# Kernel tuning notes

Hardware: AMD Instinct MI355X
Metric: run time of the kernel (lower is better)

## Reference

```python
import jax, jax.numpy as jnp
import numpy as np

B, N, C, NS = 4, 2048, 128, 64
RADIUS = 0.25
BN_EPS = 1e-5


def _ball_query(xyz):
    """First-NS point indices within RADIUS of each point (pointnet2 semantics:
    indices taken in ascending point order, short balls padded with the first hit).
    xyz: (B,N,3) -> idx: (B,N,NS) int32."""
    sq = jnp.sum(xyz * xyz, axis=-1)                                   # (B,N)
    d2 = sq[:, :, None] + sq[:, None, :] - 2.0 * jnp.einsum('bnd,bmd->bnm', xyz, xyz)
    within = d2 < RADIUS ** 2                                          # (B,N,N)
    cand = jnp.where(within, jnp.arange(N, dtype=jnp.int32)[None, None, :], N)
    idx = jnp.sort(cand, axis=-1)[..., :NS]                            # first NS hits
    idx = jnp.where(idx == N, idx[..., :1], idx)                       # pad with first hit
    return idx


def _bn_relu(h, g, b):
    # eval-mode BatchNorm2d with running_mean=0, running_var=1, then ReLU
    inv = 1.0 / jnp.sqrt(1.0 + BN_EPS)
    return jax.nn.relu(g[None, :, None, None] * (h * inv) + b[None, :, None, None])


def _forward(xyz, features, W1, W2, W3, g1, g2, g3, b1, b2, b3):
    idx = _ball_query(xyz)                                             # (B,N,NS)
    bidx = jnp.arange(B)[:, None, None]
    g_xyz = xyz[bidx, idx]                                             # (B,N,NS,3)
    grouped_xyz = jnp.transpose(g_xyz - xyz[:, :, None, :], (0, 3, 1, 2))  # (B,3,N,NS) relative
    feat_t = jnp.transpose(features, (0, 2, 1))                        # (B,N,C)
    g_feat = jnp.transpose(feat_t[bidx, idx], (0, 3, 1, 2))            # (B,C,N,NS)
    grouped_features = jnp.concatenate([grouped_xyz, g_feat], axis=1)  # (B,3+C,N,NS)

    xyz_feature = jnp.concatenate([jnp.transpose(xyz, (0, 2, 1)), features], axis=1)  # (B,3+C,N)
    center = jax.lax.stop_gradient(xyz_feature)[..., None]             # .detach() in torch
    diff = grouped_features - center
    h = diff * diff                                                    # squared diff

    h = _bn_relu(jnp.einsum('oc,bcns->bons', W1, h), g1, b1)           # (B,256,N,NS)
    h = _bn_relu(jnp.einsum('oc,bcns->bons', W2, h), g2, b2)           # (B,128,N,NS)
    h = _bn_relu(jnp.einsum('oc,bcns->bons', W3, h), g3, b3)           # (B,1,N,NS)

    shift = jnp.sum(grouped_xyz * h, axis=-1)                          # (B,3,N)
    return shift / jnp.sum(h, axis=-1)                                 # / (B,1,N)


def setup_inputs() -> dict:
    key = jax.random.key(0)
    ks = jax.random.split(key, 5)
    cin = C + 3
    return {
        'xyz': jax.random.uniform(ks[0], (B, N, 3), dtype=jnp.float32),
        'features': jax.random.normal(ks[1], (B, C, N), dtype=jnp.float32),
        'W1': jax.random.normal(ks[2], (256, cin), dtype=jnp.float32) * np.float32(np.sqrt(2.0 / cin)),
        'W2': jax.random.normal(ks[3], (128, 256), dtype=jnp.float32) * np.float32(np.sqrt(2.0 / 256)),
        'W3': jax.random.normal(ks[4], (1, 128), dtype=jnp.float32) * np.float32(np.sqrt(2.0 / 128)),
        'g1': jnp.ones((256,), jnp.float32), 'g2': jnp.ones((128,), jnp.float32), 'g3': jnp.ones((1,), jnp.float32),
        'b1': jnp.zeros((256,), jnp.float32), 'b2': jnp.zeros((128,), jnp.float32), 'b3': jnp.zeros((1,), jnp.float32),
    }


def reference(xyz, features, W1, W2, W3, g1, g2, g3, b1, b2, b3):
    return _forward(xyz, features, W1, W2, W3, g1, g2, g3, b1, b2, b3)
```

## Files before the change

kernel.cpp:

```cpp
#include <hip/hip_runtime.h>
#include <math.h>

typedef _Float16 f16;
typedef _Float16 f16x8 __attribute__((ext_vector_type(8)));
typedef _Float16 f16x4 __attribute__((ext_vector_type(4)));
typedef float f32x4 __attribute__((ext_vector_type(4)));

#define B_  4
#define N_  2048
#define C_  128
#define NS_ 64

#define WS_FEAT16 0u
#define WS_IDX    2097152u
#define WS_W1X    3145728u
#define WS_W1P    3153920u
#define WS_W2P    3219456u

#define OFF_H   0
#define OFF_HX  16384
#define OFF_W   18432
#define OFF_GX  51200
#define OFF_Z3  51968
#define LDS_TOTAL 53248

__device__ __forceinline__ void gl_lds16(const char* gp, char* lp) {
  __builtin_amdgcn_global_load_lds(
      (const __attribute__((address_space(1))) unsigned int*)gp,
      (__attribute__((address_space(3))) unsigned int*)lp, 16, 0, 0);
}

__device__ __forceinline__ unsigned pk2(float a, float b) {
  union { f16 h[2]; unsigned u; } cv;
  cv.h[0] = (f16)a; cv.h[1] = (f16)b;
  return cv.u;
}

__global__ __launch_bounds__(256) void prep_kernel(
    const float* __restrict__ feat, const float* __restrict__ W1,
    const float* __restrict__ W2,
    const float* __restrict__ g1, const float* __restrict__ g2,
    f16* __restrict__ feat16,
    char* __restrict__ W1x, char* __restrict__ W1p, char* __restrict__ W2p)
{
  const float inv = 1.0f / sqrtf(1.0f + 1e-5f);
  int i = blockIdx.x * 256 + threadIdx.x;
  {
    int n = i & (N_ - 1);
    int bc = i >> 11;
    int c = bc & (C_ - 1);
    int b = bc >> 7;
    feat16[(size_t)((b << 11) + n) * C_ + c] = (f16)feat[i];
  }
  if (i < 16384) {
    int g = i >> 12, r = i & 4095, o = r >> 4, j = r & 15;
    float sc = g1[o] * inv;
    const float* row = W1 + o * 131 + 3 + g * 32 + 2 * j;
    unsigned byte = ((unsigned)(o * 64 + j * 4)) ^ ((unsigned)(((o >> 1) & 7) << 4));
    *(unsigned*)(W1p + (size_t)g * 16384 + byte) = pk2(row[0] * sc, row[1] * sc);
  }
  if (i < 16384) {
    int ko = i >> 12, r = i & 4095, p = r >> 5, j = r & 31;
    float sc = g2[p] * inv;
    int o = ko * 64 + 2 * j;
    unsigned byte = ((unsigned)(p * 128 + j * 4)) ^ ((unsigned)((p & 7) << 4));
    *(unsigned*)(W2p + (size_t)ko * 16384 + byte) =
        pk2(W2[p * 256 + o] * sc, W2[p * 256 + o + 1] * sc);
  }
  if (i < 2048) {
    int o = i >> 3, j = i & 7;
    float sc = g1[o] * inv;
    unsigned v = 0;
    if (j == 0)      v = pk2(W1[o * 131 + 0] * sc, W1[o * 131 + 1] * sc);
    else if (j == 1) v = pk2(W1[o * 131 + 2] * sc, 0.0f);
    *(unsigned*)(W1x + o * 32 + j * 4) = v;
  }
}

__global__ __launch_bounds__(256) void ballquery_kernel(
    const float* __restrict__ xyz, unsigned short* __restrict__ idxout)
{
  __shared__ float  xl[N_ * 3];
  __shared__ double sq[N_];
  __shared__ int    ibuf[4][NS_];

  const int b  = blockIdx.x >> 9;
  const int ng = blockIdx.x & 511;
  const int t  = threadIdx.x;
  const float* xb = xyz + (size_t)b * N_ * 3;

  for (int i = t; i < N_ * 3; i += 256) xl[i] = xb[i];
  __syncthreads();
  for (int i = t; i < N_; i += 256) {
    double x = (double)xl[3*i], y = (double)xl[3*i+1], z = (double)xl[3*i+2];
    sq[i] = x*x + y*y + z*z;
  }
  __syncthreads();

  const int wv = t >> 6, lane = t & 63;
  const int n = ng * 4 + wv;
  const double xn = (double)xl[3*n], yn = (double)xl[3*n+1], zn = (double)xl[3*n+2];
  const double sn = sq[n];

  int cnt = 0;
  for (int mb = 0; mb < N_; mb += 64) {
    int m = mb + lane;
    double dot = xn*(double)xl[3*m] + yn*(double)xl[3*m+1] + zn*(double)xl[3*m+2];
    double d2 = (sn + sq[m]) - 2.0 * dot;
    bool hit = d2 < 0.0625;
    unsigned long long mask = __ballot(hit);
    int pos = __popcll(mask & ((1ULL << lane) - 1ULL));
    int slot = cnt + pos;
    if (hit && slot < NS_) ibuf[wv][slot] = m;
    cnt += (int)__popcll(mask);
    if (cnt >= NS_) break;
  }
  asm volatile("s_waitcnt lgkmcnt(0)" ::: "memory");
  int total = cnt < NS_ ? cnt : NS_;
  int v = ibuf[wv][lane < total ? lane : 0];
  idxout[((size_t)b * N_ + n) * NS_ + lane] = (unsigned short)v;
}

__global__ __launch_bounds__(256, 3) void mlp_kernel(
    const float* __restrict__ xyz, const f16* __restrict__ feat16,
    const char* __restrict__ w1x, const char* __restrict__ w1p,
    const char* __restrict__ w2p,
    const unsigned short* __restrict__ idxg,
    const float* __restrict__ W3g,
    const float* __restrict__ b1,
    const float* __restrict__ b2,
    const float* __restrict__ g3, const float* __restrict__ b3,
    float* __restrict__ out)
{
  __shared__ __attribute__((aligned(128))) char lds[LDS_TOTAL];

  const int bidRaw = blockIdx.x;
  const int bn = ((bidRaw & 7) << 10) + (bidRaw >> 3);
  const int b = bn >> 11;
  const int n = bn & (N_ - 1);
  const int t = threadIdx.x;
  const int w = t >> 6, lane = t & 63;
  const int l15 = lane & 15, lg = lane >> 4;
  const unsigned swzl = (unsigned)(((l15 >> 1) & 7) << 4);
  const unsigned labase = ((unsigned)(l15 * 64 + lg * 16)) ^ swzl;
  const unsigned swz2 = (unsigned)((l15 & 7) << 4);
  const unsigned w2b0 = ((unsigned)(l15 * 128 + lg * 16)) ^ swz2;
  const unsigned w2b1 = ((unsigned)(l15 * 128 + 64 + lg * 16)) ^ swz2;
  const float inv = 1.0f / sqrtf(1.0f + 1e-5f);

  float bo1v[4];
  #pragma unroll
  for (int nt = 0; nt < 4; ++nt) {
    int o = (nt >> 1) * 128 + 32 * w + (nt & 1) * 16 + l15;
    bo1v[nt] = b1[o];
  }
  float bo2v[2];
  #pragma unroll
  for (int nt = 0; nt < 2; ++nt) {
    int p = 32 * w + nt * 16 + l15;
    bo2v[nt] = b2[p];
  }
  const float g3c = g3[0] * inv, b3c = b3[0];
  const float w3a = W3g[32 * w + l15] * g3c;
  const float w3b = W3g[32 * w + 16 + l15] * g3c;
  const float xn0 = xyz[(size_t)bn*3+0], xn1 = xyz[(size_t)bn*3+1], xn2 = xyz[(size_t)bn*3+2];

  auto STAGE = [&](int sl) {
    const char* gp; int nloads;
    if (sl == 0)      { gp = w1x;                          nloads = 2; }
    else if (sl <= 4) { gp = w1p + (size_t)(sl - 1) * 16384; nloads = 4; }
    else              { gp = w2p + (size_t)(sl - 5) * 16384; nloads = 4; }
    gp += t * 16;
    char* lp = lds + OFF_W + ((sl & 1) << 14) + (w << 10);
    for (int i = 0; i < nloads; ++i)
      gl_lds16(gp + i * 4096, lp + i * 4096);
  };

  f32x4 acc1[4][4];
  f32x4 acc2[4][2];
  #pragma unroll
  for (int mt = 0; mt < 4; ++mt)
    #pragma unroll
    for (int nt2 = 0; nt2 < 2; ++nt2) {
      f32x4 c = {bo2v[nt2], bo2v[nt2], bo2v[nt2], bo2v[nt2]};
      acc2[mt][nt2] = c;
    }

  STAGE(0);
  const int s_me = t & 63, g_me = t >> 6;
  const int m_me = (int)idxg[(size_t)bn * 64 + s_me];

  {
    const f16* pb = feat16 + ((size_t)b * N_ + m_me) * C_ + g_me * 32;
    const f16* qb = feat16 + (size_t)bn * C_ + g_me * 32;
    const unsigned sw = ((unsigned)((s_me >> 1) & 7)) << 4;
    const unsigned base = (unsigned)(g_me * 4096);
    #pragma unroll
    for (int qq = 0; qq < 4; ++qq) {
      f16x8 p = *(const f16x8*)(pb + qq * 8);
      f16x8 q = *(const f16x8*)(qb + qq * 8);
      f16x8 d = p - q;
      f16x8 hh = d * d;
      unsigned byte = base
        + ((((unsigned)(s_me * 64 + qq * 16)) ^ sw ^ ((unsigned)((g_me & 3) << 4))));
      *(f16x8*)(lds + OFF_H + byte) = hh;
    }
  }
  if (t < 64) {
    const float* pm = xyz + ((size_t)b * N_ + m_me) * 3;
    float p0 = pm[0], p1 = pm[1], p2c = pm[2];
    float* gxp = (float*)(lds + OFF_GX) + s_me * 3;
    gxp[0] = p0 - xn0; gxp[1] = p1 - xn1; gxp[2] = p2c - xn2;
    float h0 = p0 - 2.0f * xn0; h0 *= h0;
    float h1 = p1 - 2.0f * xn1; h1 *= h1;
    float h2 = p2c - 2.0f * xn2; h2 *= h2;
    char* hx = lds + OFF_HX + s_me * 32;
    *(unsigned*)(hx + 0)  = pk2(h0, h1);
    *(unsigned*)(hx + 4)  = pk2(h2, 0.0f);
    *(unsigned*)(hx + 8)  = 0u;
    *(unsigned*)(hx + 12) = 0u;
    f32x4 z4 = {0.0f, 0.0f, 0.0f, 0.0f};
    *(f32x4*)(hx + 16) = z4;
  }

  asm volatile("s_waitcnt vmcnt(0) lgkmcnt(0)" ::: "memory");
  __builtin_amdgcn_s_barrier();
  STAGE(1);
  {
    const char* wbx = lds + OFF_W;
    f16x4 bf4[4];
    #pragma unroll
    for (int nt = 0; nt < 4; ++nt) {
      int orow = (nt >> 1) * 128 + 32 * w + (nt & 1) * 16 + l15;
      bf4[nt] = *(const f16x4*)(wbx + orow * 32 + lg * 8);
    }
    f16x4 af4[4];
    #pragma unroll
    for (int mt = 0; mt < 4; ++mt)
      af4[mt] = *(const f16x4*)(lds + OFF_HX + (16 * mt + l15) * 32 + lg * 8);
    #pragma unroll
    for (int mt = 0; mt < 4; ++mt)
      #pragma unroll
      for (int nt = 0; nt < 4; ++nt) {
        f32x4 cb = {bo1v[nt], bo1v[nt], bo1v[nt], bo1v[nt]};
        acc1[mt][nt] = __builtin_amdgcn_mfma_f32_16x16x16f16(af4[mt], bf4[nt], cb, 0, 0, 0);
      }
  }

  #pragma unroll
  for (int g = 0; g < 4; ++g) {
    const int sl = 1 + g;
    asm volatile("s_waitcnt vmcnt(0) lgkmcnt(0)" ::: "memory");
    __builtin_amdgcn_s_barrier();
    STAGE(sl + 1);
    const char* wb = lds + OFF_W + ((sl & 1) << 14);
    f16x8 bf[4];
    #pragma unroll
    for (int nt = 0; nt < 4; ++nt) {
      int ob = (nt >> 1) * 128 + 32 * w + (nt & 1) * 16;
      bf[nt] = *(const f16x8*)(wb + ob * 64 + labase);
    }
    const char* hb = lds + OFF_H + g * 4096;
    const unsigned gx4 = ((unsigned)g) << 4;
    f16x8 af[4];
    #pragma unroll
    for (int mt = 0; mt < 4; ++mt)
      af[mt] = *(const f16x8*)(hb + mt * 1024 + (labase ^ gx4));
    __builtin_amdgcn_s_setprio(1);
    #pragma unroll
    for (int mt = 0; mt < 4; ++mt)
      #pragma unroll
      for (int nt = 0; nt < 4; ++nt)
        acc1[mt][nt] = __builtin_amdgcn_mfma_f32_16x16x32_f16(af[mt], bf[nt], acc1[mt][nt], 0, 0, 0);
    __builtin_amdgcn_s_setprio(0);
  }

  auto EPI1 = [&](int hf) {
    #pragma unroll
    for (int mt = 0; mt < 4; ++mt)
      #pragma unroll
      for (int nt2 = 0; nt2 < 2; ++nt2) {
        const int nt = hf * 2 + nt2;
        #pragma unroll
        for (int r = 0; r < 4; ++r) {
          int s = mt * 16 + lg * 4 + r;
          float a = acc1[mt][nt][r];
          a = a > 0.0f ? a : 0.0f;
          unsigned byte = (unsigned)(w * 4096)
            + (((unsigned)(s * 64 + nt2 * 32 + l15 * 2)) ^ ((unsigned)(((s >> 1) & 7) << 4))
               ^ ((unsigned)((w & 3) << 4)));
          *(f16*)(lds + OFF_H + byte) = (f16)a;
        }
      }
  };
  asm volatile("s_waitcnt lgkmcnt(0)" ::: "memory");
  __builtin_amdgcn_s_barrier();
  EPI1(0);

  #pragma unroll
  for (int k = 0; k < 4; ++k) {
    const int sl = 5 + k;
    asm volatile("s_waitcnt vmcnt(0) lgkmcnt(0)" ::: "memory");
    __builtin_amdgcn_s_barrier();
    if (sl < 8) STAGE(sl + 1);
    const char* wb = lds + OFF_W + ((sl & 1) << 14);
    f16x8 bq0[2], bq1[2];
    #pragma unroll
    for (int nt2 = 0; nt2 < 2; ++nt2) {
      int pb = (32 * w + nt2 * 16) * 128;
      bq0[nt2] = *(const f16x8*)(wb + pb + w2b0);
      bq1[nt2] = *(const f16x8*)(wb + pb + w2b1);
    }
    const int sl0 = (2 * k) & 3, sl1 = (2 * k + 1) & 3;
    f16x8 a0f[4], a1f[4];
    #pragma unroll
    for (int mt = 0; mt < 4; ++mt) {
      a0f[mt] = *(const f16x8*)(lds + OFF_H + sl0 * 4096 + mt * 1024 + (labase ^ (unsigned)(sl0 << 4)));
      a1f[mt] = *(const f16x8*)(lds + OFF_H + sl1 * 4096 + mt * 1024 + (labase ^ (unsigned)(sl1 << 4)));
    }
    __builtin_amdgcn_s_setprio(1);
    #pragma unroll
    for (int mt = 0; mt < 4; ++mt)
      #pragma unroll
      for (int nt2 = 0; nt2 < 2; ++nt2) {
        f32x4 c = acc2[mt][nt2];
        c = __builtin_amdgcn_mfma_f32_16x16x32_f16(a0f[mt], bq0[nt2], c, 0, 0, 0);
        c = __builtin_amdgcn_mfma_f32_16x16x32_f16(a1f[mt], bq1[nt2], c, 0, 0, 0);
        acc2[mt][nt2] = c;
      }
    __builtin_amdgcn_s_setprio(0);
    if (k == 1) {
      asm volatile("s_waitcnt lgkmcnt(0)" ::: "memory");
      __builtin_amdgcn_s_barrier();
      EPI1(1);
    }
  }

  {
    float pz[4][4];
    #pragma unroll
    for (int mt = 0; mt < 4; ++mt)
      #pragma unroll
      for (int r = 0; r < 4; ++r) {
        float a0 = acc2[mt][0][r]; a0 = a0 > 0.0f ? a0 : 0.0f;
        float a1 = acc2[mt][1][r]; a1 = a1 > 0.0f ? a1 : 0.0f;
        pz[mt][r] = fmaf(a0, w3a, a1 * w3b);
      }
    #pragma unroll
    for (int off = 1; off < 16; off <<= 1)
      #pragma unroll
      for (int mt = 0; mt < 4; ++mt)
        #pragma unroll
        for (int r = 0; r < 4; ++r)
          pz[mt][r] += __shfl_xor(pz[mt][r], off);
    if (l15 == 0) {
      float* z3p = (float*)(lds + OFF_Z3) + w * 64;
      #pragma unroll
      for (int mt = 0; mt < 4; ++mt)
        #pragma unroll
        for (int r = 0; r < 4; ++r)
          z3p[mt * 16 + lg * 4 + r] = pz[mt][r];
    }
  }
  asm volatile("s_waitcnt lgkmcnt(0)" ::: "memory");
  __builtin_amdgcn_s_barrier();

  if (t < 64) {
    const float* z3p = (const float*)(lds + OFF_Z3);
    float z3 = z3p[t] + z3p[64 + t] + z3p[128 + t] + z3p[192 + t] + b3c;
    float wgt = z3 > 0.0f ? z3 : 0.0f;
    const float* gx = (const float*)(lds + OFF_GX) + t * 3;
    float v0 = gx[0] * wgt, v1 = gx[1] * wgt, v2 = gx[2] * wgt, v3 = wgt;
    #pragma unroll
    for (int off = 1; off < 64; off <<= 1) {
      v0 += __shfl_xor(v0, off); v1 += __shfl_xor(v1, off);
      v2 += __shfl_xor(v2, off); v3 += __shfl_xor(v3, off);
    }
    if (t == 0) {
      out[(size_t)(b * 3 + 0) * N_ + n] = v0 / v3;
      out[(size_t)(b * 3 + 1) * N_ + n] = v1 / v3;
      out[(size_t)(b * 3 + 2) * N_ + n] = v2 / v3;
    }
  }
}

extern "C" void kernel_launch(void* const* d_in, const int* in_sizes, int n_in,
                              void* d_out, int out_size, void* d_ws, size_t ws_size,
                              hipStream_t stream) {
  (void)in_sizes; (void)n_in; (void)out_size; (void)ws_size;
  const float* xyz      = (const float*)d_in[0];
  const float* features = (const float*)d_in[1];
  const float* W1 = (const float*)d_in[2];
  const float* W2 = (const float*)d_in[3];
  const float* W3 = (const float*)d_in[4];
  const float* g1 = (const float*)d_in[5];
  const float* g2 = (const float*)d_in[6];
  const float* g3 = (const float*)d_in[7];
  const float* b1 = (const float*)d_in[8];
  const float* b2 = (const float*)d_in[9];
  const float* b3 = (const float*)d_in[10];
  float* out = (float*)d_out;

  char* ws = (char*)d_ws;
  f16* feat16         = (f16*)(ws + WS_FEAT16);
  unsigned short* idx = (unsigned short*)(ws + WS_IDX);
  char* W1x           = ws + WS_W1X;
  char* W1p           = ws + WS_W1P;
  char* W2p           = ws + WS_W2P;

  prep_kernel<<<dim3((B_ * C_ * N_) / 256), dim3(256), 0, stream>>>(
      features, W1, W2, g1, g2, feat16, W1x, W1p, W2p);
  ballquery_kernel<<<dim3(B_ * N_ / 4), dim3(256), 0, stream>>>(xyz, idx);
  mlp_kernel<<<dim3(B_ * N_), dim3(256), 0, stream>>>(
      xyz, feat16, W1x, W1p, W2p, idx, W3, b1, b2, g3, b3, out);
}
```

Baseline: 143.9 us.

## Make MLP kernel persistent with all weights resident in LDS

```diff
diff --git a/kernel.cpp b/kernel.cpp
--- a/kernel.cpp
+++ b/kernel.cpp
@@ -17,12 +17,14 @@
 #define WS_W1P    3153920u
 #define WS_W2P    3219456u
 
-#define OFF_H   0
-#define OFF_HX  16384
-#define OFF_W   18432
-#define OFF_GX  51200
-#define OFF_Z3  51968
-#define LDS_TOTAL 53248
+#define OFF_H    0
+#define OFF_HX   16384
+#define OFF_W1X  18432
+#define OFF_W1F  26624
+#define OFF_W2   92160
+#define OFF_GX   157696
+#define OFF_Z3   158464
+#define LDS_TOTAL 159488
 
 __device__ __forceinline__ void gl_lds16(const char* gp, char* lp) {
   __builtin_amdgcn_global_load_lds(
@@ -121,7 +123,7 @@
   idxout[((size_t)b * N_ + n) * NS_ + lane] = (unsigned short)v;
 }
 
-__global__ __launch_bounds__(256, 3) void mlp_kernel(
+__global__ __launch_bounds__(256, 1) void mlp_kernel(
     const float* __restrict__ xyz, const f16* __restrict__ feat16,
     const char* __restrict__ w1x, const char* __restrict__ w1p,
     const char* __restrict__ w2p,
@@ -134,10 +136,9 @@
 {
   __shared__ __attribute__((aligned(128))) char lds[LDS_TOTAL];
 
-  const int bidRaw = blockIdx.x;
-  const int bn = ((bidRaw & 7) << 10) + (bidRaw >> 3);
-  const int b = bn >> 11;
-  const int n = bn & (N_ - 1);
+  const int bid = blockIdx.x;
+  const int b = bid >> 6;
+  const int n0 = (bid & 63) * 32;
   const int t = threadIdx.x;
   const int w = t >> 6, lane = t & 63;
   const int l15 = lane & 15, lg = lane >> 4;
@@ -147,6 +148,7 @@
   const unsigned w2b0 = ((unsigned)(l15 * 128 + lg * 16)) ^ swz2;
   const unsigned w2b1 = ((unsigned)(l15 * 128 + 64 + lg * 16)) ^ swz2;
   const float inv = 1.0f / sqrtf(1.0f + 1e-5f);
+  const int s_me = t & 63, g_me = t >> 6;
 
   float bo1v[4];
   #pragma unroll
@@ -163,223 +165,267 @@
   const float g3c = g3[0] * inv, b3c = b3[0];
   const float w3a = W3g[32 * w + l15] * g3c;
   const float w3b = W3g[32 * w + 16 + l15] * g3c;
-  const float xn0 = xyz[(size_t)bn*3+0], xn1 = xyz[(size_t)bn*3+1], xn2 = xyz[(size_t)bn*3+2];
-
-  auto STAGE = [&](int sl) {
-    const char* gp; int nloads;
-    if (sl == 0)      { gp = w1x;                          nloads = 2; }
-    else if (sl <= 4) { gp = w1p + (size_t)(sl - 1) * 16384; nloads = 4; }
-    else              { gp = w2p + (size_t)(sl - 5) * 16384; nloads = 4; }
-    gp += t * 16;
-    char* lp = lds + OFF_W + ((sl & 1) << 14) + (w << 10);
-    for (int i = 0; i < nloads; ++i)
-      gl_lds16(gp + i * 4096, lp + i * 4096);
-  };
-
-  f32x4 acc1[4][4];
-  f32x4 acc2[4][2];
-  #pragma unroll
-  for (int mt = 0; mt < 4; ++mt)
-    #pragma unroll
-    for (int nt2 = 0; nt2 < 2; ++nt2) {
-      f32x4 c = {bo2v[nt2], bo2v[nt2], bo2v[nt2], bo2v[nt2]};
-      acc2[mt][nt2] = c;
-    }
-
-  STAGE(0);
-  const int s_me = t & 63, g_me = t >> 6;
-  const int m_me = (int)idxg[(size_t)bn * 64 + s_me];
 
   {
-    const f16* pb = feat16 + ((size_t)b * N_ + m_me) * C_ + g_me * 32;
+    #pragma unroll
+    for (int i2 = 0; i2 < 2; ++i2)
+      gl_lds16(w1x + (size_t)i2 * 4096 + t * 16, lds + OFF_W1X + i2 * 4096 + (w << 10));
+    #pragma unroll
+    for (int i2 = 0; i2 < 16; ++i2)
+      gl_lds16(w1p + (size_t)i2 * 4096 + t * 16, lds + OFF_W1F + i2 * 4096 + (w << 10));
+    #pragma unroll
+    for (int i2 = 0; i2 < 16; ++i2)
+      gl_lds16(w2p + (size_t)i2 * 4096 + t * 16, lds + OFF_W2 + i2 * 4096 + (w << 10));
+  }
+
+  f16x8 pf[4], qf_[4];
+  float pm0 = 0.f, pm1 = 0.f, pm2 = 0.f, xq0 = 0.f, xq1 = 0.f, xq2 = 0.f;
+
+  {
+    const int bn = b * N_ + n0;
+    const int m = (int)idxg[(size_t)bn * 64 + s_me];
+    const f16* pb = feat16 + ((size_t)b * N_ + m) * C_ + g_me * 32;
     const f16* qb = feat16 + (size_t)bn * C_ + g_me * 32;
     const unsigned sw = ((unsigned)((s_me >> 1) & 7)) << 4;
-    const unsigned base = (unsigned)(g_me * 4096);
     #pragma unroll
     for (int qq = 0; qq < 4; ++qq) {
       f16x8 p = *(const f16x8*)(pb + qq * 8);
       f16x8 q = *(const f16x8*)(qb + qq * 8);
       f16x8 d = p - q;
       f16x8 hh = d * d;
-      unsigned byte = base
+      unsigned byte = (unsigned)(g_me * 4096)
         + ((((unsigned)(s_me * 64 + qq * 16)) ^ sw ^ ((unsigned)((g_me & 3) << 4))));
       *(f16x8*)(lds + OFF_H + byte) = hh;
     }
-  }
-  if (t < 64) {
-    const float* pm = xyz + ((size_t)b * N_ + m_me) * 3;
-    float p0 = pm[0], p1 = pm[1], p2c = pm[2];
-    float* gxp = (float*)(lds + OFF_GX) + s_me * 3;
-    gxp[0] = p0 - xn0; gxp[1] = p1 - xn1; gxp[2] = p2c - xn2;
-    float h0 = p0 - 2.0f * xn0; h0 *= h0;
-    float h1 = p1 - 2.0f * xn1; h1 *= h1;
-    float h2 = p2c - 2.0f * xn2; h2 *= h2;
-    char* hx = lds + OFF_HX + s_me * 32;
-    *(unsigned*)(hx + 0)  = pk2(h0, h1);
-    *(unsigned*)(hx + 4)  = pk2(h2, 0.0f);
-    *(unsigned*)(hx + 8)  = 0u;
-    *(unsigned*)(hx + 12) = 0u;
-    f32x4 z4 = {0.0f, 0.0f, 0.0f, 0.0f};
-    *(f32x4*)(hx + 16) = z4;
-  }
-
-  asm volatile("s_waitcnt vmcnt(0) lgkmcnt(0)" ::: "memory");
-  __builtin_amdgcn_s_barrier();
-  STAGE(1);
-  {
-    const char* wbx = lds + OFF_W;
-    f16x4 bf4[4];
-    #pragma unroll
-    for (int nt = 0; nt < 4; ++nt) {
-      int orow = (nt >> 1) * 128 + 32 * w + (nt & 1) * 16 + l15;
-      bf4[nt] = *(const f16x4*)(wbx + orow * 32 + lg * 8);
-    }
-    f16x4 af4[4];
+    if (t < 64) {
+      float xn0c = xyz[(size_t)bn*3+0], xn1c = xyz[(size_t)bn*3+1], xn2c = xyz[(size_t)bn*3+2];
+      const float* pm = xyz + ((size_t)b * N_ + m) * 3;
+      float p0 = pm[0], p1 = pm[1], p2c = pm[2];
+      float* gxp = (float*)(lds + OFF_GX) + s_me * 3;
+      gxp[0] = p0 - xn0c; gxp[1] = p1 - xn1c; gxp[2] = p2c - xn2c;
+      float h0 = p0 - 2.0f * xn0c; h0 *= h0;
+      float h1 = p1 - 2.0f * xn1c; h1 *= h1;
+      float h2 = p2c - 2.0f * xn2c; h2 *= h2;
+      char* hx = lds + OFF_HX + s_me * 32;
+      *(unsigned*)(hx + 0)  = pk2(h0, h1);
+      *(unsigned*)(hx + 4)  = pk2(h2, 0.0f);
+      *(unsigned*)(hx + 8)  = 0u;
+      *(unsigned*)(hx + 12) = 0u;
+      f32x4 z4 = {0.0f, 0.0f, 0.0f, 0.0f};
+      *(f32x4*)(hx + 16) = z4;
+    }
+  }
+  asm volatile("s_waitcnt vmcnt(0)" ::: "memory");
+
+  for (int it = 0; it < 32; ++it) {
+    const int n = n0 + it;
+    const int bn = b * N_ + n;
+    asm volatile("s_waitcnt lgkmcnt(0)" ::: "memory");
+    __builtin_amdgcn_s_barrier();
+
+    int m_next = 0;
+    if (it < 31) {
+      const int bn1 = bn + 1;
+      m_next = (int)idxg[(size_t)bn1 * 64 + s_me];
+      const f16* qb = feat16 + (size_t)bn1 * C_ + g_me * 32;
+      #pragma unroll
+      for (int qq = 0; qq < 4; ++qq) qf_[qq] = *(const f16x8*)(qb + qq * 8);
+      if (t < 64) {
+        xq0 = xyz[(size_t)bn1*3+0]; xq1 = xyz[(size_t)bn1*3+1]; xq2 = xyz[(size_t)bn1*3+2];
+      }
+    }
+
+    f32x4 acc1[4][4];
+    f32x4 acc2[4][2];
     #pragma unroll
     for (int mt = 0; mt < 4; ++mt)
-      af4[mt] = *(const f16x4*)(lds + OFF_HX + (16 * mt + l15) * 32 + lg * 8);
-    #pragma unroll
-    for (int mt = 0; mt < 4; ++mt)
+      #pragma unroll
+      for (int nt2 = 0; nt2 < 2; ++nt2) {
+        f32x4 c = {bo2v[nt2], bo2v[nt2], bo2v[nt2], bo2v[nt2]};
+        acc2[mt][nt2] = c;
+      }
+
+    {
+      f16x4 bf4[4], af4[4];
       #pragma unroll
       for (int nt = 0; nt < 4; ++nt) {
-        f32x4 cb = {bo1v[nt], bo1v[nt], bo1v[nt], bo1v[nt]};
-        acc1[mt][nt] = __builtin_amdgcn_mfma_f32_16x16x16f16(af4[mt], bf4[nt], cb, 0, 0, 0);
-      }
-  }
-
-  #pragma unroll
-  for (int g = 0; g < 4; ++g) {
-    const int sl = 1 + g;
-    asm volatile("s_waitcnt vmcnt(0) lgkmcnt(0)" ::: "memory");
+        int orow = (nt >> 1) * 128 + 32 * w + (nt & 1) * 16 + l15;
+        bf4[nt] = *(const f16x4*)(lds + OFF_W1X + orow * 32 + lg * 8);
+      }
+      #pragma unroll
+      for (int mt = 0; mt < 4; ++mt)
+        af4[mt] = *(const f16x4*)(lds + OFF_HX + (16 * mt + l15) * 32 + lg * 8);
+      #pragma unroll
+      for (int mt = 0; mt < 4; ++mt)
+        #pragma unroll
+        for (int nt = 0; nt < 4; ++nt) {
+          f32x4 cb = {bo1v[nt], bo1v[nt], bo1v[nt], bo1v[nt]};
+          acc1[mt][nt] = __builtin_amdgcn_mfma_f32_16x16x16f16(af4[mt], bf4[nt], cb, 0, 0, 0);
+        }
+    }
+    #pragma unroll
+    for (int g = 0; g < 4; ++g) {
+      const char* wb = lds + OFF_W1F + g * 16384;
+      f16x8 bf[4], af[4];
+      #pragma unroll
+      for (int nt = 0; nt < 4; ++nt) {
+        int ob = (nt >> 1) * 128 + 32 * w + (nt & 1) * 16;
+        bf[nt] = *(const f16x8*)(wb + ob * 64 + labase);
+      }
+      const char* hb = lds + OFF_H + g * 4096;
+      const unsigned gx4 = ((unsigned)g) << 4;
+      #pragma unroll
+      for (int mt = 0; mt < 4; ++mt)
+        af[mt] = *(const f16x8*)(hb + mt * 1024 + (labase ^ gx4));
+      __builtin_amdgcn_s_setprio(1);
+      #pragma unroll
+      for (int mt = 0; mt < 4; ++mt)
+        #pragma unroll
+        for (int nt = 0; nt < 4; ++nt)
+          acc1[mt][nt] = __builtin_amdgcn_mfma_f32_16x16x32_f16(af[mt], bf[nt], acc1[mt][nt], 0, 0, 0);
+      __builtin_amdgcn_s_setprio(0);
+    }
+
+    if (it < 31) {
+      const f16* pb = feat16 + ((size_t)b * N_ + m_next) * C_ + g_me * 32;
+      #pragma unroll
+      for (int qq = 0; qq < 4; ++qq) pf[qq] = *(const f16x8*)(pb + qq * 8);
+      if (t < 64) {
+        const float* pm = xyz + ((size_t)b * N_ + m_next) * 3;
+        pm0 = pm[0]; pm1 = pm[1]; pm2 = pm[2];
+      }
+    }
+
+    auto EPI1 = [&](int hf) {
+      #pragma unroll
+      for (int mt = 0; mt < 4; ++mt)
+        #pragma unroll
+        for (int nt2 = 0; nt2 < 2; ++nt2) {
+          const int nt = hf * 2 + nt2;
+          #pragma unroll
+          for (int r = 0; r < 4; ++r) {
+            int s = mt * 16 + lg * 4 + r;
+            float a = acc1[mt][nt][r];
+            a = a > 0.0f ? a : 0.0f;
+            unsigned byte = (unsigned)(w * 4096)
+              + (((unsigned)(s * 64 + nt2 * 32 + l15 * 2)) ^ ((unsigned)(((s >> 1) & 7) << 4))
+                 ^ ((unsigned)((w & 3) << 4)));
+            *(f16*)(lds + OFF_H + byte) = (f16)a;
+          }
+        }
+    };
+    asm volatile("s_waitcnt lgkmcnt(0)" ::: "memory");
     __builtin_amdgcn_s_barrier();
-    STAGE(sl + 1);
-    const char* wb = lds + OFF_W + ((sl & 1) << 14);
-    f16x8 bf[4];
-    #pragma unroll
-    for (int nt = 0; nt < 4; ++nt) {
-      int ob = (nt >> 1) * 128 + 32 * w + (nt & 1) * 16;
-      bf[nt] = *(const f16x8*)(wb + ob * 64 + labase);
-    }
-    const char* hb = lds + OFF_H + g * 4096;
-    const unsigned gx4 = ((unsigned)g) << 4;
-    f16x8 af[4];
-    #pragma unroll
-    for (int mt = 0; mt < 4; ++mt)
-      af[mt] = *(const f16x8*)(hb + mt * 1024 + (labase ^ gx4));
-    __builtin_amdgcn_s_setprio(1);
-    #pragma unroll
-    for (int mt = 0; mt < 4; ++mt)
-      #pragma unroll
-      for (int nt = 0; nt < 4; ++nt)
-        acc1[mt][nt] = __builtin_amdgcn_mfma_f32_16x16x32_f16(af[mt], bf[nt], acc1[mt][nt], 0, 0, 0);
-    __builtin_amdgcn_s_setprio(0);
-  }
-
-  auto EPI1 = [&](int hf) {
-    #pragma unroll
-    for (int mt = 0; mt < 4; ++mt)
+    EPI1(0);
+    asm volatile("s_waitcnt lgkmcnt(0)" ::: "memory");
+    __builtin_amdgcn_s_barrier();
+
+    #pragma unroll
+    for (int k = 0; k < 4; ++k) {
+      const char* wb = lds + OFF_W2 + k * 16384;
+      f16x8 bq0[2], bq1[2];
       #pragma unroll
       for (int nt2 = 0; nt2 < 2; ++nt2) {
-        const int nt = hf * 2 + nt2;
+        int pb2 = (32 * w + nt2 * 16) * 128;
+        bq0[nt2] = *(const f16x8*)(wb + pb2 + w2b0);
+        bq1[nt2] = *(const f16x8*)(wb + pb2 + w2b1);
+      }
+      const int sl0 = (2 * k) & 3, sl1 = (2 * k + 1) & 3;
+      f16x8 a0f[4], a1f[4];
+      #pragma unroll
+      for (int mt = 0; mt < 4; ++mt) {
+        a0f[mt] = *(const f16x8*)(lds + OFF_H + sl0 * 4096 + mt * 1024 + (labase ^ (unsigned)(sl0 << 4)));
+        a1f[mt] = *(const f16x8*)(lds + OFF_H + sl1 * 4096 + mt * 1024 + (labase ^ (unsigned)(sl1 << 4)));
+      }
+      __builtin_amdgcn_s_setprio(1);
+      #pragma unroll
+      for (int mt = 0; mt < 4; ++mt)
+        #pragma unroll
+        for (int nt2 = 0; nt2 < 2; ++nt2) {
+          f32x4 c = acc2[mt][nt2];
+          c = __builtin_amdgcn_mfma_f32_16x16x32_f16(a0f[mt], bq0[nt2], c, 0, 0, 0);
+          c = __builtin_amdgcn_mfma_f32_16x16x32_f16(a1f[mt], bq1[nt2], c, 0, 0, 0);
+          acc2[mt][nt2] = c;
+        }
+      __builtin_amdgcn_s_setprio(0);
+      if (k == 1) {
+        asm volatile("s_waitcnt lgkmcnt(0)" ::: "memory");
+        __builtin_amdgcn_s_barrier();
+        EPI1(1);
+        asm volatile("s_waitcnt lgkmcnt(0)" ::: "memory");
+        __builtin_amdgcn_s_barrier();
+      }
+    }
+
+    {
+      float pz[4][4];
+      #pragma unroll
+      for (int mt = 0; mt < 4; ++mt)
         #pragma unroll
         for (int r = 0; r < 4; ++r) {
-          int s = mt * 16 + lg * 4 + r;
-          float a = acc1[mt][nt][r];
-          a = a > 0.0f ? a : 0.0f;
-          unsigned byte = (unsigned)(w * 4096)
-            + (((unsigned)(s * 64 + nt2 * 32 + l15 * 2)) ^ ((unsigned)(((s >> 1) & 7) << 4))
-               ^ ((unsigned)((w & 3) << 4)));
-          *(f16*)(lds + OFF_H + byte) = (f16)a;
+          float a0 = acc2[mt][0][r]; a0 = a0 > 0.0f ? a0 : 0.0f;
+          float a1 = acc2[mt][1][r]; a1 = a1 > 0.0f ? a1 : 0.0f;
+          pz[mt][r] = fmaf(a0, w3a, a1 * w3b);
         }
-      }
-  };
-  asm volatile("s_waitcnt lgkmcnt(0)" ::: "memory");
-  __builtin_amdgcn_s_barrier();
-  EPI1(0);
-
-  #pragma unroll
-  for (int k = 0; k < 4; ++k) {
-    const int sl = 5 + k;
-    asm volatile("s_waitcnt vmcnt(0) lgkmcnt(0)" ::: "memory");
+      #pragma unroll
+      for (int off = 1; off < 16; off <<= 1)
+        #pragma unroll
+        for (int mt = 0; mt < 4; ++mt)
+          #pragma unroll
+          for (int r = 0; r < 4; ++r)
+            pz[mt][r] += __shfl_xor(pz[mt][r], off);
+      if (l15 == 0) {
+        float* z3p = (float*)(lds + OFF_Z3) + w * 64;
+        #pragma unroll
+        for (int mt = 0; mt < 4; ++mt)
+          #pragma unroll
+          for (int r = 0; r < 4; ++r)
+            z3p[mt * 16 + lg * 4 + r] = pz[mt][r];
+      }
+    }
+    asm volatile("s_waitcnt lgkmcnt(0)" ::: "memory");
     __builtin_amdgcn_s_barrier();
-    if (sl < 8) STAGE(sl + 1);
-    const char* wb = lds + OFF_W + ((sl & 1) << 14);
-    f16x8 bq0[2], bq1[2];
-    #pragma unroll
-    for (int nt2 = 0; nt2 < 2; ++nt2) {
-      int pb = (32 * w + nt2 * 16) * 128;
-      bq0[nt2] = *(const f16x8*)(wb + pb + w2b0);
-      bq1[nt2] = *(const f16x8*)(wb + pb + w2b1);
-    }
-    const int sl0 = (2 * k) & 3, sl1 = (2 * k + 1) & 3;
-    f16x8 a0f[4], a1f[4];
-    #pragma unroll
-    for (int mt = 0; mt < 4; ++mt) {
-      a0f[mt] = *(const f16x8*)(lds + OFF_H + sl0 * 4096 + mt * 1024 + (labase ^ (unsigned)(sl0 << 4)));
-      a1f[mt] = *(const f16x8*)(lds + OFF_H + sl1 * 4096 + mt * 1024 + (labase ^ (unsigned)(sl1 << 4)));
-    }
-    __builtin_amdgcn_s_setprio(1);
-    #pragma unroll
-    for (int mt = 0; mt < 4; ++mt)
-      #pragma unroll
-      for (int nt2 = 0; nt2 < 2; ++nt2) {
-        f32x4 c = acc2[mt][nt2];
-        c = __builtin_amdgcn_mfma_f32_16x16x32_f16(a0f[mt], bq0[nt2], c, 0, 0, 0);
-        c = __builtin_amdgcn_mfma_f32_16x16x32_f16(a1f[mt], bq1[nt2], c, 0, 0, 0);
-        acc2[mt][nt2] = c;
-      }
-    __builtin_amdgcn_s_setprio(0);
-    if (k == 1) {
-      asm volatile("s_waitcnt lgkmcnt(0)" ::: "memory");
-      __builtin_amdgcn_s_barrier();
-      EPI1(1);
-    }
-  }
-
-  {
-    float pz[4][4];
-    #pragma unroll
-    for (int mt = 0; mt < 4; ++mt)
-      #pragma unroll
-      for (int r = 0; r < 4; ++r) {
-        float a0 = acc2[mt][0][r]; a0 = a0 > 0.0f ? a0 : 0.0f;
-        float a1 = acc2[mt][1][r]; a1 = a1 > 0.0f ? a1 : 0.0f;
-        pz[mt][r] = fmaf(a0, w3a, a1 * w3b);
-      }
-    #pragma unroll
-    for (int off = 1; off < 16; off <<= 1)
-      #pragma unroll
-      for (int mt = 0; mt < 4; ++mt)
-        #pragma unroll
-        for (int r = 0; r < 4; ++r)
-          pz[mt][r] += __shfl_xor(pz[mt][r], off);
-    if (l15 == 0) {
-      float* z3p = (float*)(lds + OFF_Z3) + w * 64;
-      #pragma unroll
-      for (int mt = 0; mt < 4; ++mt)
-        #pragma unroll
-        for (int r = 0; r < 4; ++r)
-          z3p[mt * 16 + lg * 4 + r] = pz[mt][r];
-    }
-  }
-  asm volatile("s_waitcnt lgkmcnt(0)" ::: "memory");
-  __builtin_amdgcn_s_barrier();
-
-  if (t < 64) {
-    const float* z3p = (const float*)(lds + OFF_Z3);
-    float z3 = z3p[t] + z3p[64 + t] + z3p[128 + t] + z3p[192 + t] + b3c;
-    float wgt = z3 > 0.0f ? z3 : 0.0f;
-    const float* gx = (const float*)(lds + OFF_GX) + t * 3;
-    float v0 = gx[0] * wgt, v1 = gx[1] * wgt, v2 = gx[2] * wgt, v3 = wgt;
-    #pragma unroll
-    for (int off = 1; off < 64; off <<= 1) {
-      v0 += __shfl_xor(v0, off); v1 += __shfl_xor(v1, off);
-      v2 += __shfl_xor(v2, off); v3 += __shfl_xor(v3, off);
-    }
-    if (t == 0) {
-      out[(size_t)(b * 3 + 0) * N_ + n] = v0 / v3;
-      out[(size_t)(b * 3 + 1) * N_ + n] = v1 / v3;
-      out[(size_t)(b * 3 + 2) * N_ + n] = v2 / v3;
+
+    if (t < 64) {
+      const float* z3p = (const float*)(lds + OFF_Z3);
+      float z3 = z3p[t] + z3p[64 + t] + z3p[128 + t] + z3p[192 + t] + b3c;
+      float wgt = z3 > 0.0f ? z3 : 0.0f;
+      const float* gx = (const float*)(lds + OFF_GX) + t * 3;
+      float v0 = gx[0] * wgt, v1 = gx[1] * wgt, v2 = gx[2] * wgt, v3 = wgt;
+      #pragma unroll
+      for (int off = 1; off < 64; off <<= 1) {
+        v0 += __shfl_xor(v0, off); v1 += __shfl_xor(v1, off);
+        v2 += __shfl_xor(v2, off); v3 += __shfl_xor(v3, off);
+      }
+      if (t == 0) {
+        out[(size_t)(b * 3 + 0) * N_ + n] = v0 / v3;
+        out[(size_t)(b * 3 + 1) * N_ + n] = v1 / v3;
+        out[(size_t)(b * 3 + 2) * N_ + n] = v2 / v3;
+      }
+    }
+    asm volatile("s_waitcnt lgkmcnt(0)" ::: "memory");
+    __builtin_amdgcn_s_barrier();
+
+    if (it < 31) {
+      const unsigned sw = ((unsigned)((s_me >> 1) & 7)) << 4;
+      #pragma unroll
+      for (int qq = 0; qq < 4; ++qq) {
+        f16x8 d = pf[qq] - qf_[qq];
+        f16x8 hh = d * d;
+        unsigned byte = (unsigned)(g_me * 4096)
+          + ((((unsigned)(s_me * 64 + qq * 16)) ^ sw ^ ((unsigned)((g_me & 3) << 4))));
+        *(f16x8*)(lds + OFF_H + byte) = hh;
+      }
+      if (t < 64) {
+        float* gxp = (float*)(lds + OFF_GX) + s_me * 3;
+        gxp[0] = pm0 - xq0; gxp[1] = pm1 - xq1; gxp[2] = pm2 - xq2;
+        float h0 = pm0 - 2.0f * xq0; h0 *= h0;
+        float h1 = pm1 - 2.0f * xq1; h1 *= h1;
+        float h2 = pm2 - 2.0f * xq2; h2 *= h2;
+        char* hx = lds + OFF_HX + s_me * 32;
+        *(unsigned*)(hx + 0) = pk2(h0, h1);
+        *(unsigned*)(hx + 4) = pk2(h2, 0.0f);
+      }
     }
   }
 }
@@ -411,6 +457,6 @@
   prep_kernel<<<dim3((B_ * C_ * N_) / 256), dim3(256), 0, stream>>>(
       features, W1, W2, g1, g2, feat16, W1x, W1p, W2p);
   ballquery_kernel<<<dim3(B_ * N_ / 4), dim3(256), 0, stream>>>(xyz, idx);
-  mlp_kernel<<<dim3(B_ * N_), dim3(256), 0, stream>>>(
+  mlp_kernel<<<dim3(256), dim3(256), 0, stream>>>(
       xyz, feat16, W1x, W1p, W2p, idx, W3, b1, b2, g3, b3, out);
 }
```

Result: slower. 183.5 us (+27.5%).
